# Kernel tuning notes

Measured on AMD Instinct MI355X. Metric: run time of the kernel, lower is better.

The kernel has to match this reference:

```python
import jax, jax.numpy as jnp
import numpy as np

B, S, D = 4, 4096, 1024
BS = 8            # block size
N = D // BS       # num blocks = 128
K = 8             # gate levels


def _cayley_real_block(A_r, A_i):
    # A_r, A_i: [M, BS, BS]. Solve (I+A) U = (I-A) in the real 2BSx2BS isomorphism.
    M = A_r.shape[0]
    eye = jnp.eye(BS, dtype=A_r.dtype)[None]
    IpA_r = eye + A_r
    ImA_r = eye - A_r
    LHS = jnp.concatenate([
        jnp.concatenate([IpA_r, -A_i], axis=-1),
        jnp.concatenate([A_i, IpA_r], axis=-1)], axis=-2)  # [M,2BS,2BS]
    RHS = jnp.concatenate([
        jnp.concatenate([ImA_r, A_i], axis=-1),
        jnp.concatenate([-A_i, ImA_r], axis=-1)], axis=-2)
    U_rb = jnp.linalg.solve(LHS, RHS)
    return U_rb[:, :BS, :BS], U_rb[:, BS:, :BS]


def setup_inputs() -> dict:
    key = jax.random.key(0)
    k1, k2, k3, k4, k5 = jax.random.split(key, 5)
    x_real = jax.random.normal(k1, (B, S, D), dtype=jnp.float32)
    x_imag = jax.random.normal(k2, (B, S, D), dtype=jnp.float32)
    A_real = jax.random.normal(k3, (N, BS, BS), dtype=jnp.float32) * 0.02
    A_imag = jax.random.normal(k4, (N, BS, BS), dtype=jnp.float32) * 0.02
    W_gate = jax.random.normal(k5, (2 * D, D), dtype=jnp.float32) * (1.0 / np.sqrt(2 * D))
    b_gate = jnp.zeros((D,), dtype=jnp.float32)
    return {"x_real": x_real, "x_imag": x_imag, "A_real": A_real,
            "A_imag": A_imag, "W_gate": W_gate, "b_gate": b_gate}


def reference(x_real, x_imag, A_real, A_imag, W_gate, b_gate):
    # Gate: sigmoid(Linear([re, im]) * 1.7015)
    x_cat = jnp.concatenate([x_real, x_imag], axis=-1)          # [B,S,2D]
    gate = jax.nn.sigmoid((x_cat @ W_gate + b_gate) * 1.7015)    # [B,S,D]
    g_cont = gate.reshape(B, S, N, BS).mean(axis=-1)             # [B,S,N]
    level_idx = jnp.clip(jnp.round(g_cont * (K - 1)).astype(jnp.int32), 0, K - 1)
    g_levels = jnp.linspace(0.0, 1.0, K, dtype=x_real.dtype)
    g_quant = g_levels[level_idx]                                # [B,S,N]
    g_st = g_cont + jax.lax.stop_gradient(g_quant - g_cont)      # straight-through

    # Anti-Hermitian generator: skew-sym real part, sym imag part
    A_r = (A_real - jnp.swapaxes(A_real, -2, -1)) * 0.5          # [N,BS,BS]
    A_i = (A_imag + jnp.swapaxes(A_imag, -2, -1)) * 0.5

    # K*N scaled generators -> Cayley unitaries
    g_scale = g_levels[:, None, None, None]                      # [K,1,1,1]
    gA_r = (g_scale * A_r[None]).reshape(K * N, BS, BS)
    gA_i = (g_scale * A_i[None]).reshape(K * N, BS, BS)
    U_r_all, U_i_all = _cayley_real_block(gA_r, gA_i)
    U_r_all = U_r_all.reshape(K, N, BS, BS)
    U_i_all = U_i_all.reshape(K, N, BS, BS)

    # Gather per-token, per-block unitary: [B,S,N,BS,BS]
    blk = jnp.arange(N)
    U_r = U_r_all[level_idx, blk]
    U_i = U_i_all[level_idx, blk]

    xr = x_real.reshape(B, S, N, BS)
    xi = x_imag.reshape(B, S, N, BS)
    Ux_r = jnp.einsum('bsnoi,bsni->bsno', U_r, xr) - jnp.einsum('bsnoi,bsni->bsno', U_i, xi)
    Ux_i = jnp.einsum('bsnoi,bsni->bsno', U_r, xi) + jnp.einsum('bsnoi,bsni->bsno', U_i, xr)

    scale = (g_st / (g_quant + 1e-7))[..., None]                 # [B,S,N,1]
    out_r = xr + scale * (Ux_r - xr)
    out_i = xi + scale * (Ux_i - xi)
    return jax.lax.complex(out_r.reshape(B, S, D), out_i.reshape(B, S, D))
```

## Files before the change

### kernel.cpp

```cpp
#include <hip/hip_runtime.h>
#include <hip/hip_bf16.h>
#include <math.h>

#define BB 4
#define SS 4096
#define DD 1024
#define NN 128
#define KLV 8
#define MM (BB*SS)
#define NST 64

typedef short bf16x8 __attribute__((ext_vector_type(8)));
typedef float f32x4 __attribute__((ext_vector_type(4)));

__device__ unsigned short g_U16[KLV * NN * 128];
__device__ unsigned char g_levels[MM * NN];
__device__ unsigned short g_WTs[(size_t)NST * 2 * 4 * 1024 * 8];

__device__ __forceinline__ unsigned int bf16_bits(float f) {
    union { float f; unsigned int u; } v;
    v.f = f;
    unsigned int lsb = (v.u >> 16) & 1u;
    return (v.u + 0x7FFFu + lsb) >> 16;
}
__device__ __forceinline__ float bfbits2f(unsigned int b) {
    union { unsigned int u; float f; } v;
    v.u = b << 16;
    return v.f;
}

#define WT_BLOCKS (64 * 32)
__global__ __launch_bounds__(256)
void prep_kernel(const float* __restrict__ W,
                 const float* __restrict__ A_real,
                 const float* __restrict__ A_imag)
{
    __shared__ __align__(16) float sh[33 * 32];
    int blk = blockIdx.x;
    int t = threadIdx.x;

    if (blk < WT_BLOCKS) {
        float (*tile)[33] = (float(*)[33])sh;
        int bk = (blk >> 5) * 32;
        int bn = (blk & 31) * 32;

        int kk = t >> 3;
        int nn4 = (t & 7) * 4;
        float4 v = *(const float4*)&W[(size_t)(bk + kk) * DD + bn + nn4];
        tile[kk][nn4 + 0] = v.x; tile[kk][nn4 + 1] = v.y;
        tile[kk][nn4 + 2] = v.z; tile[kk][nn4 + 3] = v.w;
        __syncthreads();

        int n2 = t >> 3;
        int k4i = (t & 7) * 4;
        unsigned int hi[4], lo[4];
        #pragma unroll
        for (int q = 0; q < 4; ++q) {
            float f = tile[k4i + q][n2];
            hi[q] = bf16_bits(f);
            lo[q] = bf16_bits(f - bfbits2f(hi[q]));
        }
        int st = bk >> 5;
        int kgrp = (k4i >> 3) & 3;
        int kin = k4i & 7;
        int n = bn + n2;
        size_t bh = ((size_t)((st * 2 + 0) * 4 + kgrp) * 1024 + n) * 8 + kin;
        size_t bl = ((size_t)((st * 2 + 1) * 4 + kgrp) * 1024 + n) * 8 + kin;
        *(uint2*)&g_WTs[bh] = make_uint2(hi[0] | (hi[1] << 16), hi[2] | (hi[3] << 16));
        *(uint2*)&g_WTs[bl] = make_uint2(lo[0] | (lo[1] << 16), lo[2] | (lo[3] << 16));
        return;
    }
    blk -= WT_BLOCKS;

    {
        float (*M)[34] = (float(*)[34])sh;
        int L = blk >> 7;
        int n = blk & 127;
        float g = (float)L * (1.0f / 7.0f);

        int i = t >> 4;
        int j = t & 15;

        const float* Ar = A_real + n * 64;
        const float* Ai = A_imag + n * 64;
        int bi = i >> 3;
        int ii = i & 7, jj = j & 7;

        float ar = (Ar[ii * 8 + jj] - Ar[jj * 8 + ii]) * 0.5f * g;
        float ai = (Ai[ii * 8 + jj] + Ai[jj * 8 + ii]) * 0.5f * g;
        float eye = (ii == jj) ? 1.0f : 0.0f;

        int bj = j >> 3;
        float lhs, rhs;
        if (bi == bj) { lhs = eye + ar; rhs = eye - ar; }
        else if (bi == 0) { lhs = -ai; rhs = ai; }
        else { lhs = ai; rhs = -ai; }

        M[i][j] = lhs;
        M[i][16 + j] = rhs;
        __syncthreads();

        for (int k = 0; k < 16; ++k) {
            float f = M[i][k] / M[k][k];
            __syncthreads();
            if (i != k) {
                M[i][j]      -= f * M[k][j];
                M[i][16 + j] -= f * M[k][16 + j];
            }
            __syncthreads();
        }

        float x = M[i][16 + j] / M[i][i];
        if (j < 8) {
            g_U16[(size_t)blk * 128 + bi * 64 + ii * 8 + j] =
                (unsigned short)bf16_bits(x);
        }
    }
}

__global__ __launch_bounds__(256, 2)
void gate_v5(const float* __restrict__ xr, const float* __restrict__ xi,
             const float* __restrict__ bias)
{
    __shared__ __align__(16) unsigned short lds[8192];

    const int tid = threadIdx.x;
    const int bid = blockIdx.x;
    const int xcd = bid & 7;
    const int grp = bid >> 3;
    const int mt = xcd * 16 + (grp >> 2);
    const int nt = grp & 3;
    const int bm = mt * 128, bn = nt * 256;

    const int lane = tid & 63;
    const int wc = tid >> 6;
    const int r16 = lane & 15, sgrp = lane >> 4;

    const int arow = tid >> 1;
    const int kb = (tid & 1) * 2;

    f32x4 acc[8][4];
    #pragma unroll
    for (int a = 0; a < 8; ++a)
        #pragma unroll
        for (int b = 0; b < 4; ++b) {
            f32x4 z = {0.0f, 0.0f, 0.0f, 0.0f};
            acc[a][b] = z;
        }

    #define LOADX(dst, s)                                                         \
    {                                                                             \
        int k0_ = (s) * 32;                                                       \
        const float* src_ = (k0_ < 1024) ? xr : xi;                               \
        const float* p_ = src_ + (size_t)(bm + arow) * DD + (k0_ & 1023)          \
                          + (tid & 1) * 16;                                       \
        (dst)[0] = *(const float4*)(p_);                                          \
        (dst)[1] = *(const float4*)(p_ + 4);                                      \
        (dst)[2] = *(const float4*)(p_ + 8);                                      \
        (dst)[3] = *(const float4*)(p_ + 12);                                     \
    }

    #define WRITEA(fv, bb)                                                        \
    {                                                                             \
        float ff_[16] = {(fv)[0].x, (fv)[0].y, (fv)[0].z, (fv)[0].w,              \
                         (fv)[1].x, (fv)[1].y, (fv)[1].z, (fv)[1].w,              \
                         (fv)[2].x, (fv)[2].y, (fv)[2].z, (fv)[2].w,              \
                         (fv)[3].x, (fv)[3].y, (fv)[3].z, (fv)[3].w};             \
        unsigned int h_[16];                                                      \
        _Pragma("unroll")                                                         \
        for (int q = 0; q < 16; ++q) h_[q] = bf16_bits(ff_[q]);                   \
        _Pragma("unroll")                                                         \
        for (int b2 = 0; b2 < 2; ++b2) {                                          \
            int o_ = ((kb + b2) * 128 + arow) * 8;                                \
            *(uint4*)&lds[(bb) + o_] = make_uint4(                                \
                h_[b2*8+0] | (h_[b2*8+1] << 16), h_[b2*8+2] | (h_[b2*8+3] << 16), \
                h_[b2*8+4] | (h_[b2*8+5] << 16), h_[b2*8+6] | (h_[b2*8+7] << 16));\
        }                                                                         \
    }

    #define RA(bb, mi) (*(const bf16x8*)&lds[(bb) + \
        (sgrp * 128 + (mi) * 16 + r16) * 8])
    #define BWLD(dst, s, plane)                                                   \
    {                                                                             \
        _Pragma("unroll")                                                         \
        for (int ni = 0; ni < 4; ++ni)                                            \
            (dst)[ni] = *(const bf16x8*)&g_WTs[                                   \
                ((size_t)(((s) * 2 + (plane)) * 4 + sgrp) * 1024 +                \
                 (bn + wc * 64 + ni * 16 + r16)) * 8];                            \
    }

    #define MFMA_TERM(afr, bfr)                                                   \
    {                                                                             \
        __builtin_amdgcn_s_setprio(1);                                            \
        _Pragma("unroll")                                                         \
        for (int mi = 0; mi < 8; ++mi)                                            \
            _Pragma("unroll")                                                     \
            for (int ni = 0; ni < 4; ++ni)                                        \
                acc[mi][ni] = __builtin_amdgcn_mfma_f32_16x16x32_bf16(            \
                    (afr)[mi], (bfr)[ni], acc[mi][ni], 0, 0, 0);                  \
        __builtin_amdgcn_s_setprio(0);                                            \
    }

    bf16x8 whA[4], whB[4], wlf[4], ahi[8];
    float4 fst[4];

    #define ITER(stv, WHIN, WHOUT)                                                \
    {                                                                             \
        const int bcur_ = ((stv) & 1) * 4096;                                     \
        const int bnxt_ = bcur_ ^ 4096;                                           \
        BWLD(wlf, (stv), 1);                     \
        BWLD(WHOUT, (stv) + 1, 0);               \
        WRITEA(fst, bnxt_);                                    \
        LOADX(fst, (stv) + 2);                                 \
        _Pragma("unroll")                                                         \
        for (int mi = 0; mi < 8; ++mi) ahi[mi] = RA(bcur_, mi);                   \
        MFMA_TERM(ahi, WHIN);                                \
        MFMA_TERM(ahi, wlf);                                 \
        asm volatile("s_waitcnt lgkmcnt(0)" ::: "memory");                        \
        __builtin_amdgcn_s_barrier();                                             \
    }

    LOADX(fst, 0);
    WRITEA(fst, 0);
    LOADX(fst, 1);
    BWLD(whA, 0, 0);
    asm volatile("s_waitcnt lgkmcnt(0)" ::: "memory");
    __builtin_amdgcn_s_barrier();

    for (int st = 0; st < 62; st += 2) {
        ITER(st, whA, whB);
        ITER(st + 1, whB, whA);
    }

    {
        BWLD(wlf, 62, 1);
        BWLD(whB, 63, 0);
        WRITEA(fst, 4096);
        #pragma unroll
        for (int mi = 0; mi < 8; ++mi) ahi[mi] = RA(0, mi);
        MFMA_TERM(ahi, whA);
        MFMA_TERM(ahi, wlf);
        asm volatile("s_waitcnt lgkmcnt(0)" ::: "memory");
        __builtin_amdgcn_s_barrier();
    }
    {
        BWLD(wlf, 63, 1);
        #pragma unroll
        for (int mi = 0; mi < 8; ++mi) ahi[mi] = RA(4096, mi);
        MFMA_TERM(ahi, whB);
        MFMA_TERM(ahi, wlf);
    }
    #undef LOADX
    #undef WRITEA
    #undef RA
    #undef BWLD
    #undef MFMA_TERM
    #undef ITER

    #pragma unroll
    for (int mi = 0; mi < 8; ++mi) {
        #pragma unroll
        for (int ni = 0; ni < 4; ++ni) {
            int n = bn + wc * 64 + ni * 16 + r16;
            float bb = bias[n];
            #pragma unroll
            for (int r = 0; r < 4; ++r) {
                float z = (acc[mi][ni][r] + bb) * 1.7015f;
                float s = 1.0f / (1.0f + expf(-z));
                s += __shfl_xor(s, 1);
                s += __shfl_xor(s, 2);
                s += __shfl_xor(s, 4);
                if ((lane & 7) == 0) {
                    float gcont = s * 0.125f;
                    int lvl = (int)rintf(gcont * 7.0f);
                    lvl = min(7, max(0, lvl));
                    int m = bm + mi * 16 + sgrp * 4 + r;
                    g_levels[(size_t)m * NN + (n >> 3)] = (unsigned char)lvl;
                }
            }
        }
    }
}

__global__ __launch_bounds__(256)
void apply_kernel(const float* __restrict__ xr,
                  const float* __restrict__ xi,
                  unsigned short* __restrict__ out)
{
    int t = blockIdx.x * 256 + threadIdx.x;
    int bs = t >> 7;
    int n = t & 127;

    int L = g_levels[t];
    const unsigned short* Up = g_U16 + (size_t)(L * NN + n) * 128;
    const float* xrp = xr + (size_t)bs * DD + n * 8;
    const float* xip = xi + (size_t)bs * DD + n * 8;

    float4 r0 = *(const float4*)xrp;
    float4 r1 = *(const float4*)(xrp + 4);
    float4 i0 = *(const float4*)xip;
    float4 i1 = *(const float4*)(xip + 4);
    float xrv[8] = {r0.x, r0.y, r0.z, r0.w, r1.x, r1.y, r1.z, r1.w};
    float xiv[8] = {i0.x, i0.y, i0.z, i0.w, i1.x, i1.y, i1.z, i1.w};

    float gq = (float)L * (1.0f / 7.0f);
    float scale = gq / (gq + 1e-7f);

    unsigned int pk[8];
    #pragma unroll
    for (int oo = 0; oo < 8; ++oo) {
        uint4 uw = *(const uint4*)&Up[oo * 8];
        uint4 vw = *(const uint4*)&Up[64 + oo * 8];
        unsigned int uwa[4] = {uw.x, uw.y, uw.z, uw.w};
        unsigned int vwa[4] = {vw.x, vw.y, vw.z, vw.w};
        float ur[8], ui[8];
        #pragma unroll
        for (int q = 0; q < 4; ++q) {
            ur[2*q]   = bfbits2f(uwa[q] & 0xFFFFu);
            ur[2*q+1] = bfbits2f(uwa[q] >> 16);
            ui[2*q]   = bfbits2f(vwa[q] & 0xFFFFu);
            ui[2*q+1] = bfbits2f(vwa[q] >> 16);
        }
        float uxr = 0.0f, uxi = 0.0f;
        #pragma unroll
        for (int q = 0; q < 8; ++q) {
            uxr += ur[q] * xrv[q] - ui[q] * xiv[q];
            uxi += ur[q] * xiv[q] + ui[q] * xrv[q];
        }
        float outr = xrv[oo] + scale * (uxr - xrv[oo]);
        float outi = xiv[oo] + scale * (uxi - xiv[oo]);
        pk[oo] = bf16_bits(outi) | (bf16_bits(outr) << 16);
    }

    unsigned int* ob = (unsigned int*)(out + 2 * ((size_t)bs * DD + (size_t)n * 8));
    *(uint4*)&ob[0] = make_uint4(pk[0], pk[1], pk[2], pk[3]);
    *(uint4*)&ob[4] = make_uint4(pk[4], pk[5], pk[6], pk[7]);
}

extern "C" void kernel_launch(void* const* d_in, const int* in_sizes, int n_in,
                              void* d_out, int out_size, void* d_ws, size_t ws_size,
                              hipStream_t stream) {
    (void)in_sizes; (void)n_in; (void)out_size; (void)d_ws; (void)ws_size;
    const float* x_real = (const float*)d_in[0];
    const float* x_imag = (const float*)d_in[1];
    const float* A_real = (const float*)d_in[2];
    const float* A_imag = (const float*)d_in[3];
    const float* W_gate = (const float*)d_in[4];
    const float* b_gate = (const float*)d_in[5];
    unsigned short* out = (unsigned short*)d_out;

    hipLaunchKernelGGL(prep_kernel, dim3(WT_BLOCKS + KLV * NN), dim3(256),
                       0, stream, W_gate, A_real, A_imag);
    hipLaunchKernelGGL(gate_v5, dim3(512), dim3(256), 0, stream,
                       x_real, x_imag, b_gate);
    hipLaunchKernelGGL(apply_kernel, dim3((MM * NN) / 256), dim3(256), 0, stream,
                       x_real, x_imag, out);
}
```

Baseline: 232.4 us.

## Halve gate GEMM M-tile to 64 rows and raise occupancy to three blocks

The gate GEMM block tile drops from 128x256 to 64x256, doubling the grid to 1024 blocks and shrinking the accumulators and LDS buffer so launch bounds can target three blocks per CU. The register-rotating W-fragment prefetch for the next stage is removed, and both W planes are now loaded inside each iteration. The aim is more concurrent waves to hide global-load latency on 256 CUs. The cost is half the A-tile reuse per W fetch, which doubles W reads from global/L2, and less software pipelining of the W loads.

```diff
diff --git a/kernel.cpp b/kernel.cpp
--- a/kernel.cpp
+++ b/kernel.cpp
@@ -118,30 +118,30 @@
     }
 }
 
-__global__ __launch_bounds__(256, 2)
-void gate_v5(const float* __restrict__ xr, const float* __restrict__ xi,
+__global__ __launch_bounds__(256, 3)
+void gate_v6(const float* __restrict__ xr, const float* __restrict__ xi,
              const float* __restrict__ bias)
 {
-    __shared__ __align__(16) unsigned short lds[8192];
+    __shared__ __align__(16) unsigned short lds[4096];
 
     const int tid = threadIdx.x;
     const int bid = blockIdx.x;
     const int xcd = bid & 7;
     const int grp = bid >> 3;
-    const int mt = xcd * 16 + (grp >> 2);
+    const int mt = xcd * 32 + (grp >> 2);
     const int nt = grp & 3;
-    const int bm = mt * 128, bn = nt * 256;
+    const int bm = mt * 64, bn = nt * 256;
 
     const int lane = tid & 63;
     const int wc = tid >> 6;
     const int r16 = lane & 15, sgrp = lane >> 4;
 
-    const int arow = tid >> 1;
-    const int kb = (tid & 1) * 2;
-
-    f32x4 acc[8][4];
+    const int arow = tid >> 2;
+    const int seg = tid & 3;
+
+    f32x4 acc[4][4];
     #pragma unroll
-    for (int a = 0; a < 8; ++a)
+    for (int a = 0; a < 4; ++a)
         #pragma unroll
         for (int b = 0; b < 4; ++b) {
             f32x4 z = {0.0f, 0.0f, 0.0f, 0.0f};
@@ -153,33 +153,25 @@
         int k0_ = (s) * 32;                                                       \
         const float* src_ = (k0_ < 1024) ? xr : xi;                               \
         const float* p_ = src_ + (size_t)(bm + arow) * DD + (k0_ & 1023)          \
-                          + (tid & 1) * 16;                                       \
+                          + seg * 8;                                              \
         (dst)[0] = *(const float4*)(p_);                                          \
         (dst)[1] = *(const float4*)(p_ + 4);                                      \
-        (dst)[2] = *(const float4*)(p_ + 8);                                      \
-        (dst)[3] = *(const float4*)(p_ + 12);                                     \
     }
 
     #define WRITEA(fv, bb)                                                        \
     {                                                                             \
-        float ff_[16] = {(fv)[0].x, (fv)[0].y, (fv)[0].z, (fv)[0].w,              \
-                         (fv)[1].x, (fv)[1].y, (fv)[1].z, (fv)[1].w,              \
-                         (fv)[2].x, (fv)[2].y, (fv)[2].z, (fv)[2].w,              \
-                         (fv)[3].x, (fv)[3].y, (fv)[3].z, (fv)[3].w};             \
-        unsigned int h_[16];                                                      \
+        float ff_[8] = {(fv)[0].x, (fv)[0].y, (fv)[0].z, (fv)[0].w,               \
+                        (fv)[1].x, (fv)[1].y, (fv)[1].z, (fv)[1].w};              \
+        unsigned int h_[8];                                                       \
         _Pragma("unroll")                                                         \
-        for (int q = 0; q < 16; ++q) h_[q] = bf16_bits(ff_[q]);                   \
-        _Pragma("unroll")                                                         \
-        for (int b2 = 0; b2 < 2; ++b2) {                                          \
-            int o_ = ((kb + b2) * 128 + arow) * 8;                                \
-            *(uint4*)&lds[(bb) + o_] = make_uint4(                                \
-                h_[b2*8+0] | (h_[b2*8+1] << 16), h_[b2*8+2] | (h_[b2*8+3] << 16), \
-                h_[b2*8+4] | (h_[b2*8+5] << 16), h_[b2*8+6] | (h_[b2*8+7] << 16));\
-        }                                                                         \
+        for (int q = 0; q < 8; ++q) h_[q] = bf16_bits(ff_[q]);                    \
+        *(uint4*)&lds[(bb) + (seg * 64 + arow) * 8] = make_uint4(                 \
+            h_[0] | (h_[1] << 16), h_[2] | (h_[3] << 16),                         \
+            h_[4] | (h_[5] << 16), h_[6] | (h_[7] << 16));                        \
     }
 
     #define RA(bb, mi) (*(const bf16x8*)&lds[(bb) + \
-        (sgrp * 128 + (mi) * 16 + r16) * 8])
+        (sgrp * 64 + (mi) * 16 + r16) * 8])
     #define BWLD(dst, s, plane)                                                   \
     {                                                                             \
         _Pragma("unroll")                                                         \
@@ -193,7 +185,7 @@
     {                                                                             \
         __builtin_amdgcn_s_setprio(1);                                            \
         _Pragma("unroll")                                                         \
-        for (int mi = 0; mi < 8; ++mi)                                            \
+        for (int mi = 0; mi < 4; ++mi)                                            \
             _Pragma("unroll")                                                     \
             for (int ni = 0; ni < 4; ++ni)                                        \
                 acc[mi][ni] = __builtin_amdgcn_mfma_f32_16x16x32_bf16(            \
@@ -201,53 +193,49 @@
         __builtin_amdgcn_s_setprio(0);                                            \
     }
 
-    bf16x8 whA[4], whB[4], wlf[4], ahi[8];
-    float4 fst[4];
-
-    #define ITER(stv, WHIN, WHOUT)                                                \
-    {                                                                             \
-        const int bcur_ = ((stv) & 1) * 4096;                                     \
-        const int bnxt_ = bcur_ ^ 4096;                                           \
-        BWLD(wlf, (stv), 1);                     \
-        BWLD(WHOUT, (stv) + 1, 0);               \
-        WRITEA(fst, bnxt_);                                    \
-        LOADX(fst, (stv) + 2);                                 \
-        _Pragma("unroll")                                                         \
-        for (int mi = 0; mi < 8; ++mi) ahi[mi] = RA(bcur_, mi);                   \
-        MFMA_TERM(ahi, WHIN);                                \
-        MFMA_TERM(ahi, wlf);                                 \
-        asm volatile("s_waitcnt lgkmcnt(0)" ::: "memory");                        \
-        __builtin_amdgcn_s_barrier();                                             \
-    }
+    bf16x8 whf[4], wlf[4], ahi[4];
+    float4 fst[2];
 
     LOADX(fst, 0);
     WRITEA(fst, 0);
     LOADX(fst, 1);
-    BWLD(whA, 0, 0);
     asm volatile("s_waitcnt lgkmcnt(0)" ::: "memory");
     __builtin_amdgcn_s_barrier();
 
-    for (int st = 0; st < 62; st += 2) {
-        ITER(st, whA, whB);
-        ITER(st + 1, whB, whA);
-    }
-
+    for (int st = 0; st < 62; ++st) {
+        const int bcur = (st & 1) * 2048;
+        const int bnxt = bcur ^ 2048;
+
+        BWLD(whf, st, 0);
+        BWLD(wlf, st, 1);
+        WRITEA(fst, bnxt);
+        LOADX(fst, st + 2);
+
+        #pragma unroll
+        for (int mi = 0; mi < 4; ++mi) ahi[mi] = RA(bcur, mi);
+        MFMA_TERM(ahi, whf);
+        MFMA_TERM(ahi, wlf);
+
+        asm volatile("s_waitcnt lgkmcnt(0)" ::: "memory");
+        __builtin_amdgcn_s_barrier();
+    }
     {
+        BWLD(whf, 62, 0);
         BWLD(wlf, 62, 1);
-        BWLD(whB, 63, 0);
-        WRITEA(fst, 4096);
-        #pragma unroll
-        for (int mi = 0; mi < 8; ++mi) ahi[mi] = RA(0, mi);
-        MFMA_TERM(ahi, whA);
+        WRITEA(fst, 2048);
+        #pragma unroll
+        for (int mi = 0; mi < 4; ++mi) ahi[mi] = RA(0, mi);
+        MFMA_TERM(ahi, whf);
         MFMA_TERM(ahi, wlf);
         asm volatile("s_waitcnt lgkmcnt(0)" ::: "memory");
         __builtin_amdgcn_s_barrier();
     }
     {
+        BWLD(whf, 63, 0);
         BWLD(wlf, 63, 1);
         #pragma unroll
-        for (int mi = 0; mi < 8; ++mi) ahi[mi] = RA(4096, mi);
-        MFMA_TERM(ahi, whB);
+        for (int mi = 0; mi < 4; ++mi) ahi[mi] = RA(2048, mi);
+        MFMA_TERM(ahi, whf);
         MFMA_TERM(ahi, wlf);
     }
     #undef LOADX
@@ -255,10 +243,9 @@
     #undef RA
     #undef BWLD
     #undef MFMA_TERM
-    #undef ITER
 
     #pragma unroll
-    for (int mi = 0; mi < 8; ++mi) {
+    for (int mi = 0; mi < 4; ++mi) {
         #pragma unroll
         for (int ni = 0; ni < 4; ++ni) {
             int n = bn + wc * 64 + ni * 16 + r16;
@@ -351,7 +338,7 @@
 
     hipLaunchKernelGGL(prep_kernel, dim3(WT_BLOCKS + KLV * NN), dim3(256),
                        0, stream, W_gate, A_real, A_imag);
-    hipLaunchKernelGGL(gate_v5, dim3(512), dim3(256), 0, stream,
+    hipLaunchKernelGGL(gate_v6, dim3(1024), dim3(256), 0, stream,
                        x_real, x_imag, b_gate);
     hipLaunchKernelGGL(apply_kernel, dim3((MM * NN) / 256), dim3(256), 0, stream,
                        x_real, x_imag, out);
```

After: 241.6 us. +4.0%, slower.

## Process two K-steps per barrier with doubled LDS staging in gate GEMM

Applied to the files above, without the earlier changes.

Restructures the gate GEMM main loop so that each iteration stages and consumes two 32-wide K slices, doubling the LDS buffer to hold two sub-tiles per stage. This halves the number of block-wide barriers and deepens the global prefetch to four steps ahead using two register staging sets. The W fragments are now loaded just before use, with no cross-iteration prefetch, which may expose global load latency. It also raises LDS use and register pressure, which could hurt occupancy at two blocks per CU. Out-of-range prefetches are clamped to the last slice.

```diff
diff --git a/kernel.cpp b/kernel.cpp
--- a/kernel.cpp
+++ b/kernel.cpp
@@ -119,10 +119,10 @@
 }
 
 __global__ __launch_bounds__(256, 2)
-void gate_v5(const float* __restrict__ xr, const float* __restrict__ xi,
+void gate_v7(const float* __restrict__ xr, const float* __restrict__ xi,
              const float* __restrict__ bias)
 {
-    __shared__ __align__(16) unsigned short lds[8192];
+    __shared__ __align__(16) unsigned short lds[16384];
 
     const int tid = threadIdx.x;
     const int bid = blockIdx.x;
@@ -150,7 +150,8 @@
 
     #define LOADX(dst, s)                                                         \
     {                                                                             \
-        int k0_ = (s) * 32;                                                       \
+        int s_ = (s) > 63 ? 63 : (s);                                             \
+        int k0_ = s_ * 32;                                                        \
         const float* src_ = (k0_ < 1024) ? xr : xi;                               \
         const float* p_ = src_ + (size_t)(bm + arow) * DD + (k0_ & 1023)          \
                           + (tid & 1) * 16;                                       \
@@ -160,7 +161,7 @@
         (dst)[3] = *(const float4*)(p_ + 12);                                     \
     }
 
-    #define WRITEA(fv, bb)                                                        \
+    #define WRITEA(fv, bb, sub)                                                   \
     {                                                                             \
         float ff_[16] = {(fv)[0].x, (fv)[0].y, (fv)[0].z, (fv)[0].w,              \
                          (fv)[1].x, (fv)[1].y, (fv)[1].z, (fv)[1].w,              \
@@ -171,14 +172,14 @@
         for (int q = 0; q < 16; ++q) h_[q] = bf16_bits(ff_[q]);                   \
         _Pragma("unroll")                                                         \
         for (int b2 = 0; b2 < 2; ++b2) {                                          \
-            int o_ = ((kb + b2) * 128 + arow) * 8;                                \
-            *(uint4*)&lds[(bb) + o_] = make_uint4(                                \
+            int o_ = (bb) + (sub) * 4096 + ((kb + b2) * 128 + arow) * 8;          \
+            *(uint4*)&lds[o_] = make_uint4(                                       \
                 h_[b2*8+0] | (h_[b2*8+1] << 16), h_[b2*8+2] | (h_[b2*8+3] << 16), \
                 h_[b2*8+4] | (h_[b2*8+5] << 16), h_[b2*8+6] | (h_[b2*8+7] << 16));\
         }                                                                         \
     }
 
-    #define RA(bb, mi) (*(const bf16x8*)&lds[(bb) + \
+    #define RA(bb, sub, mi) (*(const bf16x8*)&lds[(bb) + (sub) * 4096 + \
         (sgrp * 128 + (mi) * 16 + r16) * 8])
     #define BWLD(dst, s, plane)                                                   \
     {                                                                             \
@@ -201,61 +202,50 @@
         __builtin_amdgcn_s_setprio(0);                                            \
     }
 
-    bf16x8 whA[4], whB[4], wlf[4], ahi[8];
-    float4 fst[4];
-
-    #define ITER(stv, WHIN, WHOUT)                                                \
-    {                                                                             \
-        const int bcur_ = ((stv) & 1) * 4096;                                     \
-        const int bnxt_ = bcur_ ^ 4096;                                           \
-        BWLD(wlf, (stv), 1);                     \
-        BWLD(WHOUT, (stv) + 1, 0);               \
-        WRITEA(fst, bnxt_);                                    \
-        LOADX(fst, (stv) + 2);                                 \
-        _Pragma("unroll")                                                         \
-        for (int mi = 0; mi < 8; ++mi) ahi[mi] = RA(bcur_, mi);                   \
-        MFMA_TERM(ahi, WHIN);                                \
-        MFMA_TERM(ahi, wlf);                                 \
-        asm volatile("s_waitcnt lgkmcnt(0)" ::: "memory");                        \
-        __builtin_amdgcn_s_barrier();                                             \
-    }
-
-    LOADX(fst, 0);
-    WRITEA(fst, 0);
-    LOADX(fst, 1);
-    BWLD(whA, 0, 0);
+    bf16x8 whf[4], wlf[4], ahi[8];
+    float4 fs0[4], fs1[4];
+
+    LOADX(fs0, 0);
+    LOADX(fs1, 1);
+    WRITEA(fs0, 0, 0);
+    WRITEA(fs1, 0, 1);
+    LOADX(fs0, 2);
+    LOADX(fs1, 3);
     asm volatile("s_waitcnt lgkmcnt(0)" ::: "memory");
     __builtin_amdgcn_s_barrier();
 
-    for (int st = 0; st < 62; st += 2) {
-        ITER(st, whA, whB);
-        ITER(st + 1, whB, whA);
-    }
-
-    {
-        BWLD(wlf, 62, 1);
-        BWLD(whB, 63, 0);
-        WRITEA(fst, 4096);
-        #pragma unroll
-        for (int mi = 0; mi < 8; ++mi) ahi[mi] = RA(0, mi);
-        MFMA_TERM(ahi, whA);
+    for (int t = 0; t < 32; ++t) {
+        const int bcur = (t & 1) * 8192;
+        const int bnxt = bcur ^ 8192;
+        const int s0 = 2 * t, s1 = 2 * t + 1;
+
+        WRITEA(fs0, bnxt, 0);
+        WRITEA(fs1, bnxt, 1);
+        LOADX(fs0, s0 + 4);
+        LOADX(fs1, s1 + 4);
+
+        BWLD(whf, s0, 0);
+        BWLD(wlf, s0, 1);
+        #pragma unroll
+        for (int mi = 0; mi < 8; ++mi) ahi[mi] = RA(bcur, 0, mi);
+        MFMA_TERM(ahi, whf);
         MFMA_TERM(ahi, wlf);
+
+        BWLD(whf, s1, 0);
+        BWLD(wlf, s1, 1);
+        #pragma unroll
+        for (int mi = 0; mi < 8; ++mi) ahi[mi] = RA(bcur, 1, mi);
+        MFMA_TERM(ahi, whf);
+        MFMA_TERM(ahi, wlf);
+
         asm volatile("s_waitcnt lgkmcnt(0)" ::: "memory");
         __builtin_amdgcn_s_barrier();
-    }
-    {
-        BWLD(wlf, 63, 1);
-        #pragma unroll
-        for (int mi = 0; mi < 8; ++mi) ahi[mi] = RA(4096, mi);
-        MFMA_TERM(ahi, whB);
-        MFMA_TERM(ahi, wlf);
     }
     #undef LOADX
     #undef WRITEA
     #undef RA
     #undef BWLD
     #undef MFMA_TERM
-    #undef ITER
 
     #pragma unroll
     for (int mi = 0; mi < 8; ++mi) {
@@ -351,7 +341,7 @@
 
     hipLaunchKernelGGL(prep_kernel, dim3(WT_BLOCKS + KLV * NN), dim3(256),
                        0, stream, W_gate, A_real, A_imag);
-    hipLaunchKernelGGL(gate_v5, dim3(512), dim3(256), 0, stream,
+    hipLaunchKernelGGL(gate_v7, dim3(512), dim3(256), 0, stream,
                        x_real, x_imag, b_gate);
     hipLaunchKernelGGL(apply_kernel, dim3((MM * NN) / 256), dim3(256), 0, stream,
                        x_real, x_imag, out);
```

Measured after the change: 235.0 us. About the same (+1.1%).
